# Kernel tuning notes

Measured on AMD Instinct MI355X. Metric: run time of the kernel, lower is better.

## Reference

```python
import jax, jax.numpy as jnp
import numpy as np

B, M, K, F_IN, H = 64, 1024, 16, 4, 64  # B graphs of M nodes each, k=16 neighbors


def _knn_idx(h):
    # h: [B, M, H] -> indices of K nearest neighbors (excluding self): [B, M, K]
    sq = jnp.sum(h * h, axis=-1)                                   # [B, M]
    d = sq[:, :, None] + sq[:, None, :] - 2.0 * jnp.einsum('bmf,bnf->bmn', h, h)
    d = jnp.where(jnp.eye(M, dtype=bool)[None], jnp.float32(jnp.inf), d)
    _, idx = jax.lax.top_k(-d, K)                                  # smallest distances
    return idx


def _edge_conv(h, w1, b1, w2, b2):
    # Dynamic-graph EdgeConv with max aggregation (PyG default):
    # msg = MLP(concat[x_i, x_j - x_i]); out_i = max_j msg
    idx = _knn_idx(h)                                              # [B, M, K]
    x_j = jax.vmap(lambda hb, ib: hb[ib])(h, idx)                  # [B, M, K, H]
    x_i = jnp.broadcast_to(h[:, :, None, :], x_j.shape)
    msg = jnp.concatenate([x_i, x_j - x_i], axis=-1)               # [B, M, K, 2H]
    msg = jax.nn.relu(msg @ w1 + b1) @ w2 + b2                     # [B, M, K, H]
    return jnp.max(msg, axis=2)                                    # [B, M, H]


def setup_inputs() -> dict:
    key = jax.random.key(0)
    ks = jax.random.split(key, 20)

    def lin(k, fi, fo):
        return jax.random.normal(k, (fi, fo), jnp.float32) / np.sqrt(fi)

    inp = {
        'x': jax.random.normal(ks[0], (B * M, F_IN), jnp.float32),
        'batch': jnp.repeat(jnp.arange(B, dtype=jnp.int64), M),
        # encoder: Linear(4,32) ReLU Linear(32,64) ReLU
        'enc_w1': lin(ks[1], F_IN, 32), 'enc_b1': jnp.zeros((32,), jnp.float32),
        'enc_w2': lin(ks[2], 32, H),    'enc_b2': jnp.zeros((H,), jnp.float32),
        # EdgeConv MLPs: Linear(128,64) ReLU Linear(64,64)
        'ec1_w1': lin(ks[3], 2 * H, H), 'ec1_b1': jnp.zeros((H,), jnp.float32),
        'ec1_w2': lin(ks[4], H, H),     'ec1_b2': jnp.zeros((H,), jnp.float32),
        'ec2_w1': lin(ks[5], 2 * H, H), 'ec2_b1': jnp.zeros((H,), jnp.float32),
        'ec2_w2': lin(ks[6], H, H),     'ec2_b2': jnp.zeros((H,), jnp.float32),
        # output MLP: Linear(64,32) ReLU Linear(32,1)
        'out_w1': lin(ks[7], H, 32),    'out_b1': jnp.zeros((32,), jnp.float32),
        'out_w2': lin(ks[8], 32, 1),    'out_b2': jnp.zeros((1,), jnp.float32),
    }
    return inp


def reference(x, batch, enc_w1, enc_b1, enc_w2, enc_b2,
              ec1_w1, ec1_b1, ec1_w2, ec1_b2,
              ec2_w1, ec2_b1, ec2_w2, ec2_b2,
              out_w1, out_b1, out_w2, out_b2):
    # batch is repeat(arange(B), M): equal-size graphs -> reshape into [B, M, .]
    h = jax.nn.relu(jax.nn.relu(x @ enc_w1 + enc_b1) @ enc_w2 + enc_b2)  # [N, 64]
    h = h.reshape(B, M, H)
    h = _edge_conv(h, ec1_w1, ec1_b1, ec1_w2, ec1_b2)
    h = _edge_conv(h, ec2_w1, ec2_b1, ec2_w2, ec2_b2)
    g = jnp.mean(h, axis=1)                                        # global_mean_pool -> [B, 64]
    out = jax.nn.relu(g @ out_w1 + out_b1) @ out_w2 + out_b2       # [B, 1]
    return out.reshape(-1)                                         # [B]
```

## Files before the change

### kernel.cpp

```cpp
#include <hip/hip_runtime.h>
#include <math.h>

#define B_ 64
#define M_ 1024
#define H_ 64
#define N_ (B_*M_)

typedef _Float16 half8 __attribute__((ext_vector_type(8)));
typedef float  floatx4 __attribute__((ext_vector_type(4)));

#define MFMA16(a,b,c) __builtin_amdgcn_mfma_f32_16x16x32_f16(a,b,c,0,0,0)
#define MED3(a,b,c)   __builtin_amdgcn_fmed3f(a,b,c)

__global__ __launch_bounds__(256) void enc_kernel(
    const float* __restrict__ x,
    const float* __restrict__ w1,
    const float* __restrict__ b1,
    const float* __restrict__ w2,
    const float* __restrict__ b2,
    float* __restrict__ h,
    _Float16* __restrict__ hhi,
    _Float16* __restrict__ hlo,
    float* __restrict__ sq)
{
    __shared__ float sw1[4*32];
    __shared__ float sb1[32];
    __shared__ float sw2[32*64];
    __shared__ float sb2[64];
    int t = threadIdx.x;
    for (int i = t; i < 128; i += 256) sw1[i] = w1[i];
    if (t < 32) sb1[t] = b1[t];
    for (int i = t; i < 2048; i += 256) sw2[i] = w2[i];
    if (t < 64) sb2[t] = b2[t];
    __syncthreads();
    int n = blockIdx.x * 256 + t;
    float4 xv = *(const float4*)(x + (size_t)n*4);
    float hid[32];
    #pragma unroll
    for (int o = 0; o < 32; ++o) {
        float a = sb1[o] + xv.x*sw1[0*32+o] + xv.y*sw1[1*32+o]
                        + xv.z*sw1[2*32+o] + xv.w*sw1[3*32+o];
        hid[o] = fmaxf(a, 0.f);
    }
    float* hout = h + (size_t)n*64;
    float sqa = 0.f;
    #pragma unroll 4
    for (int oc = 0; oc < 16; ++oc) {
        float4 acc = make_float4(sb2[oc*4+0], sb2[oc*4+1], sb2[oc*4+2], sb2[oc*4+3]);
        #pragma unroll
        for (int f = 0; f < 32; ++f) {
            float4 w = *(const float4*)(sw2 + f*64 + oc*4);
            float hv = hid[f];
            acc.x += hv*w.x; acc.y += hv*w.y; acc.z += hv*w.z; acc.w += hv*w.w;
        }
        acc.x = fmaxf(acc.x,0.f); acc.y = fmaxf(acc.y,0.f);
        acc.z = fmaxf(acc.z,0.f); acc.w = fmaxf(acc.w,0.f);
        *(float4*)(hout + oc*4) = acc;
        sqa += acc.x*acc.x + acc.y*acc.y + acc.z*acc.z + acc.w*acc.w;
        union { _Float16 f[4]; uint2 u; } Hh, Hl;
        Hh.f[0]=(_Float16)acc.x; Hh.f[1]=(_Float16)acc.y;
        Hh.f[2]=(_Float16)acc.z; Hh.f[3]=(_Float16)acc.w;
        Hl.f[0]=(_Float16)(acc.x-(float)Hh.f[0]); Hl.f[1]=(_Float16)(acc.y-(float)Hh.f[1]);
        Hl.f[2]=(_Float16)(acc.z-(float)Hh.f[2]); Hl.f[3]=(_Float16)(acc.w-(float)Hh.f[3]);
        *(uint2*)(hhi + (size_t)n*64 + oc*4) = Hh.u;
        *(uint2*)(hlo + (size_t)n*64 + oc*4) = Hl.u;
    }
    sq[n] = sqa;
}

__global__ __launch_bounds__(256) void convert_kernel(
    const float* __restrict__ h,
    _Float16* __restrict__ hhi, _Float16* __restrict__ hlo,
    float* __restrict__ sq)
{
    int t = threadIdx.x, lane = t & 63, w = t >> 6;
    int base = blockIdx.x * 64 + w * 16;
    for (int it = 0; it < 16; ++it) {
        int i = base + it;
        float v = h[(size_t)i*64 + lane];
        _Float16 hi = (_Float16)v;
        _Float16 lo = (_Float16)(v - (float)hi);
        hhi[(size_t)i*64 + lane] = hi;
        hlo[(size_t)i*64 + lane] = lo;
        float s = v*v;
        #pragma unroll
        for (int off = 1; off < 64; off <<= 1) s += __shfl_xor(s, off, 64);
        if (lane == 0) sq[i] = s;
    }
}

__global__ __launch_bounds__(256) void gemmA_kernel(
    const float* __restrict__ h,
    const float* __restrict__ w1,
    float* __restrict__ A)
{
    __shared__ float sw[64*64];
    int t = threadIdx.x;
    for (int idx = t; idx < 4096; idx += 256) sw[idx] = w1[4096 + idx];
    __syncthreads();
    int n = blockIdx.x * 256 + t;
    float4 hv[16];
    const float* src = h + (size_t)n*64;
    #pragma unroll
    for (int c = 0; c < 16; ++c) hv[c] = *(const float4*)(src + c*4);
    float* dst = A + (size_t)n*64;
    #pragma unroll 2
    for (int oc = 0; oc < 16; ++oc) {
        float4 acc = make_float4(0.f,0.f,0.f,0.f);
        #pragma unroll
        for (int f = 0; f < 64; ++f) {
            float xv = ((const float*)hv)[f];
            float4 w = *(const float4*)(sw + f*64 + oc*4);
            acc.x += xv*w.x; acc.y += xv*w.y; acc.z += xv*w.z; acc.w += xv*w.w;
        }
        *(float4*)(dst + oc*4) = acc;
    }
}

__global__ __launch_bounds__(256, 2) void knn_kernel(
    const _Float16* __restrict__ hhi,
    const _Float16* __restrict__ hlo,
    const float* __restrict__ sqg,
    unsigned short* __restrict__ knn)
{
    __shared__ __align__(16) _Float16 bufH[2][32*64];
    __shared__ __align__(16) _Float16 bufL[2][32*64];
    __shared__ __align__(16) float sqS[1024];
    __shared__ float md[128*65];

    int t = threadIdx.x, lane = t & 63, w = t >> 6;
    int bi = blockIdx.x;
    int g   = (bi & 7) | ((bi >> 6) << 3);
    int qt8 = (bi >> 3) & 7;
    const _Float16* hhig = hhi + (size_t)g*M_*64;
    const _Float16* hlog = hlo + (size_t)g*M_*64;
    const float*    sqb  = sqg + (size_t)g*M_;

    ((float4*)sqS)[t] = ((const float4*)sqb)[t];

    int m16 = lane & 15, gid = lane >> 4;
    int crow = gid*4, koct = gid*8;
    int sw = m16 & 7;

    int u  = ((w & 1) << 6) | lane;
    int rr = u >> 3;
    int gl = u & 7;
    int pp = gl ^ (rr & 7);
    const _Float16* srcb = (w < 2 ? hhig : hlog) + rr*64 + gl*8;
    _Float16* dst0 = (w < 2 ? bufH[0] : bufL[0]) + rr*64 + pp*8;
    _Float16* dst1 = (w < 2 ? bufH[1] : bufL[1]) + rr*64 + pp*8;

    int qbase = qt8*128 + w*32;
    half8 Q0h0, Q0h1, Q0l0, Q0l1, Q1h0, Q1h1, Q1l0, Q1l1;
    {
        const _Float16* ph = hhig + (size_t)(qbase + m16)*64;
        const _Float16* pl = hlog + (size_t)(qbase + m16)*64;
        Q0h0 = *(const half8*)(ph + koct);
        Q0h1 = *(const half8*)(ph + 32 + koct);
        Q0l0 = *(const half8*)(pl + koct);
        Q0l1 = *(const half8*)(pl + 32 + koct);
        ph += 16*64; pl += 16*64;
        Q1h0 = *(const half8*)(ph + koct);
        Q1h1 = *(const half8*)(ph + 32 + koct);
        Q1l0 = *(const half8*)(pl + koct);
        Q1l1 = *(const half8*)(pl + 32 + koct);
    }

    float bd0[16], bd1[16];
    #pragma unroll
    for (int k = 0; k < 16; ++k) { bd0[k] = INFINITY; bd1[k] = INFINITY; }

    int ts0 = qt8*8 + w*2;
    int ts1 = ts0 + 1;

    float4 a0, a1, b0, b1;
    a0 = *(const float4*)(srcb);
    a1 = *(const float4*)(srcb + 1024);
    b0 = *(const float4*)(srcb + 2048);
    b1 = *(const float4*)(srcb + 3072);
    *(float4*)dst0 = a0;  *(float4*)(dst0 + 1024) = a1;
    a0 = *(const float4*)(srcb + 2*2048);
    a1 = *(const float4*)(srcb + 2*2048 + 1024);
    __syncthreads();

    float c10 = 1.f + sqS[qbase + m16];
    float c11 = 1.f + sqS[qbase + 16 + m16];

    int o0 = m16*64 + ((gid ^ sw) * 8);
    int o1 = o0 ^ 32;

    auto insert4 = [&](float (&bdr)[16], floatx4 acc, float4 sqv,
                       unsigned cid, bool st, float c1v) {
        #pragma unroll
        for (int r = 0; r < 4; ++r) {
            float s  = fmaf(-2.f, acc[r], (&sqv.x)[r]);
            float t2 = c1v + s;
            unsigned kb = (__float_as_uint(t2) & 0xFFFFFC00u) | (cid + r);
            float fk = __uint_as_float(kb);
            if (st && (crow + r) == m16) fk = INFINITY;
            float nb0 = fminf(bdr[0], fk);
            #pragma unroll
            for (int k = 15; k >= 1; --k) bdr[k] = MED3(fk, bdr[k-1], bdr[k]);
            bdr[0] = nb0;
        }
    };

    auto compute = [&](int T, const _Float16* bh, const _Float16* bl) {
        #pragma unroll
        for (int s = 0; s < 2; ++s) {
            int ob = s*1024;
            half8 Ah0 = *(const half8*)(bh + ob + o0);
            half8 Ah1 = *(const half8*)(bh + ob + o1);
            half8 Al0 = *(const half8*)(bl + ob + o0);
            half8 Al1 = *(const half8*)(bl + ob + o1);
            float4 sqv = *(const float4*)(sqS + T*32 + s*16 + crow);
            unsigned cid = (unsigned)(T*32 + s*16 + crow);
            int ts = T*2 + s;
            floatx4 acc = {0.f, 0.f, 0.f, 0.f};
            acc = MFMA16(Ah0, Q0h0, acc);
            acc = MFMA16(Ah1, Q0h1, acc);
            acc = MFMA16(Ah0, Q0l0, acc);
            acc = MFMA16(Ah1, Q0l1, acc);
            acc = MFMA16(Al0, Q0h0, acc);
            acc = MFMA16(Al1, Q0h1, acc);
            insert4(bd0, acc, sqv, cid, ts == ts0, c10);
            floatx4 acc2 = {0.f, 0.f, 0.f, 0.f};
            acc2 = MFMA16(Ah0, Q1h0, acc2);
            acc2 = MFMA16(Ah1, Q1h1, acc2);
            acc2 = MFMA16(Ah0, Q1l0, acc2);
            acc2 = MFMA16(Ah1, Q1l1, acc2);
            acc2 = MFMA16(Al0, Q1h0, acc2);
            acc2 = MFMA16(Al1, Q1h1, acc2);
            insert4(bd1, acc2, sqv, cid, ts == ts1, c11);
        }
    };

    #pragma unroll 1
    for (int T = 0; T < 32; T += 2) {
        __builtin_amdgcn_s_barrier();
        *(float4*)dst1 = b0;  *(float4*)(dst1 + 1024) = b1;
        { size_t o = (size_t)((T+3)&31)*2048;
          b0 = *(const float4*)(srcb + o);
          b1 = *(const float4*)(srcb + o + 1024); }
        asm volatile("s_waitcnt lgkmcnt(0)" ::: "memory");
        __builtin_amdgcn_s_barrier();
        __builtin_amdgcn_sched_barrier(0);
        compute(T, bufH[0], bufL[0]);
        __builtin_amdgcn_s_barrier();
        *(float4*)dst0 = a0;  *(float4*)(dst0 + 1024) = a1;
        { size_t o = (size_t)((T+4)&31)*2048;
          a0 = *(const float4*)(srcb + o);
          a1 = *(const float4*)(srcb + o + 1024); }
        asm volatile("s_waitcnt lgkmcnt(0)" ::: "memory");
        __builtin_amdgcn_s_barrier();
        __builtin_amdgcn_sched_barrier(0);
        compute(T+1, bufH[1], bufL[1]);
    }

    __syncthreads();
    int qrow0 = w*32 + m16;
    #pragma unroll
    for (int k = 0; k < 16; ++k) {
        md[qrow0*65 + gid*16 + k]      = bd0[k];
        md[(qrow0+16)*65 + gid*16 + k] = bd1[k];
    }
    __syncthreads();
    if (w < 2) {
        int q = w*64 + lane;
        float b2[16];
        #pragma unroll
        for (int k = 0; k < 16; ++k) b2[k] = INFINITY;
        const float* mrow = md + (size_t)q*65;
        #pragma unroll
        for (int c8 = 0; c8 < 8; ++c8) {
            float sv[8];
            #pragma unroll
            for (int j = 0; j < 8; ++j) sv[j] = mrow[c8*8 + j];
            #pragma unroll
            for (int j = 0; j < 8; ++j) {
                float s = sv[j];
                float nb0 = fminf(b2[0], s);
                #pragma unroll
                for (int k = 15; k >= 1; --k) b2[k] = MED3(s, b2[k-1], b2[k]);
                b2[0] = nb0;
            }
        }
        union { unsigned short us[16]; uint4 v4[2]; } o;
        #pragma unroll
        for (int k = 0; k < 16; ++k)
            o.us[k] = (unsigned short)(__float_as_uint(b2[k]) & 1023u);
        size_t gq = (size_t)g*M_ + qt8*128 + q;
        uint4* dst = (uint4*)(knn + gq*16);
        dst[0] = o.v4[0];
        dst[1] = o.v4[1];
    }
}

__global__ __launch_bounds__(256) void edge_kernel(
    const float* __restrict__ h,
    const float* __restrict__ A,
    const unsigned short* __restrict__ knn,
    const float* __restrict__ w1,
    const float* __restrict__ b1,
    const float* __restrict__ w2,
    const float* __restrict__ b2,
    float* __restrict__ hout,
    float* __restrict__ gsum)
{
    __shared__ __align__(16) _Float16 wdf[16*64*8];
    __shared__ __align__(16) _Float16 w2f[16*64*8];
    float* CsB = (float*)w2f;
    int t = threadIdx.x;
    for (int u = t; u < 512; u += 256) {
        int ulane = u & 63, nt = u >> 7, ks = (u >> 6) & 1;
        int n = nt*16 + (ulane & 15);
        int kbase = ks*32 + ((ulane >> 4) * 8);
        int fh = (((nt*2+ks)*2+0)*64 + ulane)*8;
        int fl = (((nt*2+ks)*2+1)*64 + ulane)*8;
        #pragma unroll
        for (int j = 0; j < 8; ++j) {
            int k = kbase + j;
            float vd = w1[k*64+n] - w1[4096 + k*64+n];
            _Float16 dh = (_Float16)vd;
            wdf[fh+j] = dh;
            wdf[fl+j] = (_Float16)(vd - (float)dh);
            float v2 = w2[k*64+n];
            _Float16 h2 = (_Float16)v2;
            w2f[fh+j] = h2;
            w2f[fl+j] = (_Float16)(v2 - (float)h2);
        }
    }
    __syncthreads();
    int lane = t & 63, wid = t >> 6;
    int m16 = lane & 15, gid = lane >> 4;
    int koct = gid*8, crow = gid*4;
    int bi = blockIdx.x;
    int g  = (bi & 7) | ((bi >> 7) << 3);
    int qt = (bi >> 3) & 15;
    int i0 = g*M_ + qt*64 + wid*16;
    const float* Ab = A + (size_t)g*M_*H_;

    half8 W2r[4][2][2];
    #pragma unroll
    for (int nt = 0; nt < 4; ++nt)
        #pragma unroll
        for (int ks = 0; ks < 2; ++ks)
            #pragma unroll
            for (int p = 0; p < 2; ++p)
                W2r[nt][ks][p] = *(const half8*)&w2f[(((nt*2+ks)*2+p)*64+lane)*8];

    float b1v[4];
    #pragma unroll
    for (int nt = 0; nt < 4; ++nt) b1v[nt] = b1[nt*16+m16];
    float b2v = b2[gid*16+m16];
    __syncthreads();

    half8 Hh[2], Hl[2];
    #pragma unroll
    for (int ks = 0; ks < 2; ++ks) {
        const float* hp = h + (size_t)(i0+m16)*64 + ks*32 + koct;
        float4 v0 = *(const float4*)hp;
        float4 v1 = *(const float4*)(hp+4);
        float va[8] = {v0.x,v0.y,v0.z,v0.w,v1.x,v1.y,v1.z,v1.w};
        #pragma unroll
        for (int j = 0; j < 8; ++j) {
            _Float16 hi = (_Float16)va[j];
            Hh[ks][j] = hi;
            Hl[ks][j] = (_Float16)(va[j]-(float)hi);
        }
    }
    #pragma unroll
    for (int nt = 0; nt < 4; ++nt) {
        floatx4 acc = {b1v[nt], b1v[nt], b1v[nt], b1v[nt]};
        #pragma unroll
        for (int ks = 0; ks < 2; ++ks) {
            half8 wh = *(const half8*)&wdf[(((nt*2+ks)*2+0)*64+lane)*8];
            half8 wl = *(const half8*)&wdf[(((nt*2+ks)*2+1)*64+lane)*8];
            acc = MFMA16(Hh[ks], wh, acc);
            acc = MFMA16(Hh[ks], wl, acc);
            acc = MFMA16(Hl[ks], wh, acc);
        }
        #pragma unroll
        for (int r = 0; r < 4; ++r)
            CsB[((wid*16) + crow + r)*64 + nt*16 + m16] = acc[r];
    }
    __syncthreads();

    const unsigned short* knb = knn + (size_t)i0*16;
    float ssum = 0.f;
    #pragma unroll 2
    for (int nn = 0; nn < 16; ++nn) {
        int j = knb[nn*16 + m16];
        const float* Ap = Ab + (size_t)j*64;
        half8 Mh[2], Ml[2];
        #pragma unroll
        for (int ks = 0; ks < 2; ++ks) {
            float4 a0 = *(const float4*)(Ap + ks*32 + koct);
            float4 a1 = *(const float4*)(Ap + ks*32 + koct + 4);
            const float* cp = &CsB[(wid*16 + nn)*64 + ks*32 + koct];
            float4 c0 = *(const float4*)cp;
            float4 c1 = *(const float4*)(cp+4);
            float mv[8] = {
                fmaxf(a0.x+c0.x,0.f), fmaxf(a0.y+c0.y,0.f),
                fmaxf(a0.z+c0.z,0.f), fmaxf(a0.w+c0.w,0.f),
                fmaxf(a1.x+c1.x,0.f), fmaxf(a1.y+c1.y,0.f),
                fmaxf(a1.z+c1.z,0.f), fmaxf(a1.w+c1.w,0.f)};
            #pragma unroll
            for (int jj = 0; jj < 8; ++jj) {
                _Float16 hi = (_Float16)mv[jj];
                Mh[ks][jj] = hi;
                Ml[ks][jj] = (_Float16)(mv[jj]-(float)hi);
            }
        }
        floatx4 acc[4];
        #pragma unroll
        for (int nt = 0; nt < 4; ++nt) {
            acc[nt] = (floatx4){0.f,0.f,0.f,0.f};
            #pragma unroll
            for (int ks = 0; ks < 2; ++ks) {
                acc[nt] = MFMA16(Mh[ks], W2r[nt][ks][0], acc[nt]);
                acc[nt] = MFMA16(Mh[ks], W2r[nt][ks][1], acc[nt]);
                acc[nt] = MFMA16(Ml[ks], W2r[nt][ks][0], acc[nt]);
            }
        }
        float om[4];
        #pragma unroll
        for (int nt = 0; nt < 4; ++nt) {
            float mr = fmaxf(fmaxf(acc[nt][0], acc[nt][1]),
                             fmaxf(acc[nt][2], acc[nt][3]));
            mr = fmaxf(mr, __shfl_xor(mr, 16, 64));
            mr = fmaxf(mr, __shfl_xor(mr, 32, 64));
            om[nt] = mr;
        }
        float val = (gid == 0) ? om[0] : (gid == 1) ? om[1]
                  : (gid == 2) ? om[2] : om[3];
        float outv = val + b2v;
        if (gsum) ssum += outv;
        else hout[(size_t)(i0+nn)*64 + gid*16 + m16] = outv;
    }

    if (gsum) {
        float* part = (float*)wdf;
        part[wid*64 + gid*16 + m16] = ssum;
        __syncthreads();
        if (t < 64) {
            float tot = part[t] + part[64+t] + part[128+t] + part[192+t];
            gsum[(size_t)(g*16 + qt)*64 + t] = tot;
        }
    }
}

__global__ __launch_bounds__(64) void poolf_kernel(
    const float* __restrict__ gsum,
    const float* __restrict__ w1,
    const float* __restrict__ b1,
    const float* __restrict__ w2,
    const float* __restrict__ b2,
    float* __restrict__ out)
{
    __shared__ float g[64];
    __shared__ float hid[32];
    int t = threadIdx.x;
    int b = blockIdx.x;
    float s = 0.f;
    #pragma unroll
    for (int k = 0; k < 16; ++k) s += gsum[(size_t)(b*16 + k)*64 + t];
    g[t] = s * (1.f/M_);
    __syncthreads();
    if (t < 32) {
        float a = b1[t];
        for (int f = 0; f < 64; ++f) a += g[f] * w1[f*32 + t];
        hid[t] = fmaxf(a, 0.f);
    }
    __syncthreads();
    if (t == 0) {
        float a = b2[0];
        for (int f = 0; f < 32; ++f) a += hid[f] * w2[f];
        out[b] = a;
    }
}

extern "C" void kernel_launch(void* const* d_in, const int* in_sizes, int n_in,
                              void* d_out, int out_size, void* d_ws, size_t ws_size,
                              hipStream_t stream)
{
    (void)in_sizes; (void)n_in; (void)out_size; (void)ws_size;
    const float* x      = (const float*)d_in[0];
    const float* enc_w1 = (const float*)d_in[2];
    const float* enc_b1 = (const float*)d_in[3];
    const float* enc_w2 = (const float*)d_in[4];
    const float* enc_b2 = (const float*)d_in[5];
    const float* ec1_w1 = (const float*)d_in[6];
    const float* ec1_b1 = (const float*)d_in[7];
    const float* ec1_w2 = (const float*)d_in[8];
    const float* ec1_b2 = (const float*)d_in[9];
    const float* ec2_w1 = (const float*)d_in[10];
    const float* ec2_b1 = (const float*)d_in[11];
    const float* ec2_w2 = (const float*)d_in[12];
    const float* ec2_b2 = (const float*)d_in[13];
    const float* out_w1 = (const float*)d_in[14];
    const float* out_b1 = (const float*)d_in[15];
    const float* out_w2 = (const float*)d_in[16];
    const float* out_b2 = (const float*)d_in[17];

    char* ws = (char*)d_ws;
    float*          h   = (float*)(ws);
    char*           r2  = ws + (size_t)N_*64*4;
    _Float16*       hhi = (_Float16*)r2;
    _Float16*       hlo = (_Float16*)(r2 + (size_t)N_*64*2);
    float*          A   = (float*)r2;
    unsigned short* idx = (unsigned short*)(ws + (size_t)N_*64*4*2);
    float*          sq  = (float*)(ws + (size_t)N_*64*4*2 + (size_t)N_*16*2);
    float*          gsum = sq;

    enc_kernel<<<N_/256, 256, 0, stream>>>(x, enc_w1, enc_b1, enc_w2, enc_b2,
                                           h, hhi, hlo, sq);
    knn_kernel <<<B_*8, 256, 0, stream>>>(hhi, hlo, sq, idx);
    gemmA_kernel<<<N_/256, 256, 0, stream>>>(h, ec1_w1, A);
    edge_kernel<<<N_/64, 256, 0, stream>>>(h, A, idx, ec1_w1, ec1_b1, ec1_w2, ec1_b2,
                                           h, nullptr);
    convert_kernel<<<N_/64, 256, 0, stream>>>(h, hhi, hlo, sq);
    knn_kernel <<<B_*8, 256, 0, stream>>>(hhi, hlo, sq, idx);
    gemmA_kernel<<<N_/256, 256, 0, stream>>>(h, ec2_w1, A);
    edge_kernel<<<N_/64, 256, 0, stream>>>(h, A, idx, ec2_w1, ec2_b1, ec2_w2, ec2_b2,
                                           h, gsum);
    poolf_kernel<<<B_, 64, 0, stream>>>(gsum, out_w1, out_b1, out_w2, out_b2,
                                        (float*)d_out);
}
```

Measured before the change: 355.8 us.

## Drop fp32 activations, fuse conversion into edge kernel, use MFMA for gemmA

Stores node features only as fp16 hi/lo split pairs and stops writing the fp32 copy. The fp16 split and squared-norm computation move into the first edge_kernel's epilogue, which removes the separate convert_kernel launch. gemmA now runs on 16x16x32 MFMA using split-precision hi/lo products instead of scalar FP32 FMAs. The aim is less global memory traffic, one fewer launch and faster projection. The cost is an in-kernel shuffle reduction for sq and reliance on split-fp16 accuracy in gemmA.

```diff
diff --git a/kernel.cpp b/kernel.cpp
--- a/kernel.cpp
+++ b/kernel.cpp
@@ -18,7 +18,6 @@
     const float* __restrict__ b1,
     const float* __restrict__ w2,
     const float* __restrict__ b2,
-    float* __restrict__ h,
     _Float16* __restrict__ hhi,
     _Float16* __restrict__ hlo,
     float* __restrict__ sq)
@@ -42,7 +41,6 @@
                         + xv.z*sw1[2*32+o] + xv.w*sw1[3*32+o];
         hid[o] = fmaxf(a, 0.f);
     }
-    float* hout = h + (size_t)n*64;
     float sqa = 0.f;
     #pragma unroll 4
     for (int oc = 0; oc < 16; ++oc) {
@@ -55,7 +53,6 @@
         }
         acc.x = fmaxf(acc.x,0.f); acc.y = fmaxf(acc.y,0.f);
         acc.z = fmaxf(acc.z,0.f); acc.w = fmaxf(acc.w,0.f);
-        *(float4*)(hout + oc*4) = acc;
         sqa += acc.x*acc.x + acc.y*acc.y + acc.z*acc.z + acc.w*acc.w;
         union { _Float16 f[4]; uint2 u; } Hh, Hl;
         Hh.f[0]=(_Float16)acc.x; Hh.f[1]=(_Float16)acc.y;
@@ -68,52 +65,58 @@
     sq[n] = sqa;
 }
 
-__global__ __launch_bounds__(256) void convert_kernel(
-    const float* __restrict__ h,
-    _Float16* __restrict__ hhi, _Float16* __restrict__ hlo,
-    float* __restrict__ sq)
-{
-    int t = threadIdx.x, lane = t & 63, w = t >> 6;
-    int base = blockIdx.x * 64 + w * 16;
-    for (int it = 0; it < 16; ++it) {
-        int i = base + it;
-        float v = h[(size_t)i*64 + lane];
-        _Float16 hi = (_Float16)v;
-        _Float16 lo = (_Float16)(v - (float)hi);
-        hhi[(size_t)i*64 + lane] = hi;
-        hlo[(size_t)i*64 + lane] = lo;
-        float s = v*v;
-        #pragma unroll
-        for (int off = 1; off < 64; off <<= 1) s += __shfl_xor(s, off, 64);
-        if (lane == 0) sq[i] = s;
-    }
-}
-
 __global__ __launch_bounds__(256) void gemmA_kernel(
-    const float* __restrict__ h,
+    const _Float16* __restrict__ hhi,
+    const _Float16* __restrict__ hlo,
     const float* __restrict__ w1,
     float* __restrict__ A)
 {
-    __shared__ float sw[64*64];
+    __shared__ __align__(16) _Float16 wf[16*64*8];
     int t = threadIdx.x;
-    for (int idx = t; idx < 4096; idx += 256) sw[idx] = w1[4096 + idx];
-    __syncthreads();
-    int n = blockIdx.x * 256 + t;
-    float4 hv[16];
-    const float* src = h + (size_t)n*64;
-    #pragma unroll
-    for (int c = 0; c < 16; ++c) hv[c] = *(const float4*)(src + c*4);
-    float* dst = A + (size_t)n*64;
-    #pragma unroll 2
-    for (int oc = 0; oc < 16; ++oc) {
-        float4 acc = make_float4(0.f,0.f,0.f,0.f);
-        #pragma unroll
-        for (int f = 0; f < 64; ++f) {
-            float xv = ((const float*)hv)[f];
-            float4 w = *(const float4*)(sw + f*64 + oc*4);
-            acc.x += xv*w.x; acc.y += xv*w.y; acc.z += xv*w.z; acc.w += xv*w.w;
-        }
-        *(float4*)(dst + oc*4) = acc;
+    for (int u = t; u < 512; u += 256) {
+        int ulane = u & 63, nt = u >> 7, ks = (u >> 6) & 1;
+        int n = nt*16 + (ulane & 15);
+        int kbase = ks*32 + ((ulane >> 4) * 8);
+        int fh = (((nt*2+ks)*2+0)*64 + ulane)*8;
+        int fl = (((nt*2+ks)*2+1)*64 + ulane)*8;
+        #pragma unroll
+        for (int j = 0; j < 8; ++j) {
+            int k = kbase + j;
+            float v = w1[4096 + k*64 + n];
+            _Float16 hi = (_Float16)v;
+            wf[fh+j] = hi;
+            wf[fl+j] = (_Float16)(v - (float)hi);
+        }
+    }
+    __syncthreads();
+    int lane = t & 63, wid = t >> 6;
+    int m16 = lane & 15, gid = lane >> 4;
+    int koct = gid*8, crow = gid*4;
+    int n0 = blockIdx.x*256 + wid*64;
+    #pragma unroll
+    for (int ng = 0; ng < 4; ++ng) {
+        int nb = n0 + ng*16;
+        half8 Hh[2], Hl[2];
+        #pragma unroll
+        for (int ks = 0; ks < 2; ++ks) {
+            Hh[ks] = *(const half8*)(hhi + (size_t)(nb+m16)*64 + ks*32 + koct);
+            Hl[ks] = *(const half8*)(hlo + (size_t)(nb+m16)*64 + ks*32 + koct);
+        }
+        #pragma unroll
+        for (int nt = 0; nt < 4; ++nt) {
+            floatx4 acc = {0.f,0.f,0.f,0.f};
+            #pragma unroll
+            for (int ks = 0; ks < 2; ++ks) {
+                half8 wh = *(const half8*)&wf[(((nt*2+ks)*2+0)*64+lane)*8];
+                half8 wl = *(const half8*)&wf[(((nt*2+ks)*2+1)*64+lane)*8];
+                acc = MFMA16(Hh[ks], wh, acc);
+                acc = MFMA16(Hh[ks], wl, acc);
+                acc = MFMA16(Hl[ks], wh, acc);
+            }
+            #pragma unroll
+            for (int r = 0; r < 4; ++r)
+                A[(size_t)(nb+crow+r)*64 + nt*16 + m16] = acc[r];
+        }
     }
 }
 
@@ -297,14 +300,15 @@
 }
 
 __global__ __launch_bounds__(256) void edge_kernel(
-    const float* __restrict__ h,
+    _Float16* hhi,
+    _Float16* hlo,
     const float* __restrict__ A,
     const unsigned short* __restrict__ knn,
     const float* __restrict__ w1,
     const float* __restrict__ b1,
     const float* __restrict__ w2,
     const float* __restrict__ b2,
-    float* __restrict__ hout,
+    float* __restrict__ sqout,
     float* __restrict__ gsum)
 {
     __shared__ __align__(16) _Float16 wdf[16*64*8];
@@ -358,16 +362,8 @@
     half8 Hh[2], Hl[2];
     #pragma unroll
     for (int ks = 0; ks < 2; ++ks) {
-        const float* hp = h + (size_t)(i0+m16)*64 + ks*32 + koct;
-        float4 v0 = *(const float4*)hp;
-        float4 v1 = *(const float4*)(hp+4);
-        float va[8] = {v0.x,v0.y,v0.z,v0.w,v1.x,v1.y,v1.z,v1.w};
-        #pragma unroll
-        for (int j = 0; j < 8; ++j) {
-            _Float16 hi = (_Float16)va[j];
-            Hh[ks][j] = hi;
-            Hl[ks][j] = (_Float16)(va[j]-(float)hi);
-        }
+        Hh[ks] = *(const half8*)(hhi + (size_t)(i0+m16)*64 + ks*32 + koct);
+        Hl[ks] = *(const half8*)(hlo + (size_t)(i0+m16)*64 + ks*32 + koct);
     }
     #pragma unroll
     for (int nt = 0; nt < 4; ++nt) {
@@ -435,8 +431,17 @@
         float val = (gid == 0) ? om[0] : (gid == 1) ? om[1]
                   : (gid == 2) ? om[2] : om[3];
         float outv = val + b2v;
-        if (gsum) ssum += outv;
-        else hout[(size_t)(i0+nn)*64 + gid*16 + m16] = outv;
+        if (gsum) {
+            ssum += outv;
+        } else {
+            _Float16 hi = (_Float16)outv;
+            hhi[(size_t)(i0+nn)*64 + gid*16 + m16] = hi;
+            hlo[(size_t)(i0+nn)*64 + gid*16 + m16] = (_Float16)(outv - (float)hi);
+            float s2 = outv*outv;
+            #pragma unroll
+            for (int off = 1; off < 64; off <<= 1) s2 += __shfl_xor(s2, off, 64);
+            if (lane == 0) sqout[i0+nn] = s2;
+        }
     }
 
     if (gsum) {
@@ -504,26 +509,25 @@
     const float* out_b2 = (const float*)d_in[17];
 
     char* ws = (char*)d_ws;
-    float*          h   = (float*)(ws);
-    char*           r2  = ws + (size_t)N_*64*4;
-    _Float16*       hhi = (_Float16*)r2;
-    _Float16*       hlo = (_Float16*)(r2 + (size_t)N_*64*2);
-    float*          A   = (float*)r2;
+    float*          A   = (float*)(ws);
+    _Float16*       hhi = (_Float16*)(ws + (size_t)N_*64*4);
+    _Float16*       hlo = (_Float16*)(ws + (size_t)N_*64*4 + (size_t)N_*64*2);
     unsigned short* idx = (unsigned short*)(ws + (size_t)N_*64*4*2);
     float*          sq  = (float*)(ws + (size_t)N_*64*4*2 + (size_t)N_*16*2);
     float*          gsum = sq;
 
     enc_kernel<<<N_/256, 256, 0, stream>>>(x, enc_w1, enc_b1, enc_w2, enc_b2,
-                                           h, hhi, hlo, sq);
+                                           hhi, hlo, sq);
     knn_kernel <<<B_*8, 256, 0, stream>>>(hhi, hlo, sq, idx);
-    gemmA_kernel<<<N_/256, 256, 0, stream>>>(h, ec1_w1, A);
-    edge_kernel<<<N_/64, 256, 0, stream>>>(h, A, idx, ec1_w1, ec1_b1, ec1_w2, ec1_b2,
-                                           h, nullptr);
-    convert_kernel<<<N_/64, 256, 0, stream>>>(h, hhi, hlo, sq);
+    gemmA_kernel<<<N_/256, 256, 0, stream>>>(hhi, hlo, ec1_w1, A);
+    edge_kernel<<<N_/64, 256, 0, stream>>>(hhi, hlo, A, idx,
+                                           ec1_w1, ec1_b1, ec1_w2, ec1_b2,
+                                           sq, nullptr);
     knn_kernel <<<B_*8, 256, 0, stream>>>(hhi, hlo, sq, idx);
-    gemmA_kernel<<<N_/256, 256, 0, stream>>>(h, ec2_w1, A);
-    edge_kernel<<<N_/64, 256, 0, stream>>>(h, A, idx, ec2_w1, ec2_b1, ec2_w2, ec2_b2,
-                                           h, gsum);
+    gemmA_kernel<<<N_/256, 256, 0, stream>>>(hhi, hlo, ec2_w1, A);
+    edge_kernel<<<N_/64, 256, 0, stream>>>(hhi, hlo, A, idx,
+                                           ec2_w1, ec2_b1, ec2_w2, ec2_b2,
+                                           nullptr, gsum);
     poolf_kernel<<<B_, 64, 0, stream>>>(gsum, out_w1, out_b1, out_w2, out_b2,
                                         (float*)d_out);
 }
```

Result: no change. 355.6 us (-0.1%).
